# Performance work log

Hardware: AMD Instinct MI355X
Metric: run time of the kernel (lower is better)

Reference implementation:

```python
import jax, jax.numpy as jnp
import numpy as np

L = 8192   # query length
N = 8192   # key/value length
DK = 128   # head dim = dmodel // h = 2048 // 16
PAD = 128  # number of trailing padded key positions


def setup_inputs() -> dict:
    key = jax.random.key(0)
    kq, kk, kv = jax.random.split(key, 3)
    Q = jax.random.normal(kq, (L, DK), dtype=jnp.float32)
    K = jax.random.normal(kk, (N, DK), dtype=jnp.float32)
    V = jax.random.normal(kv, (N, DK), dtype=jnp.float32)
    # True = masked. Causal mask (strict upper triangle) for self-attention.
    mask_self_attention = ~jnp.tril(jnp.ones((L, N), dtype=bool))
    # Padding mask: last PAD key positions are padding.
    mask_padding = jnp.zeros((L, N), dtype=bool).at[:, N - PAD:].set(True)
    return {"Q": Q, "K": K, "V": V,
            "mask_self_attention": mask_self_attention,
            "mask_padding": mask_padding}


def reference(Q, K, V, mask_self_attention, mask_padding):
    # SDPA(Q,K,V) = softmax(QK^T / sqrt(dk)) V ; dropout is identity in eval.
    scale = 1.0 / np.sqrt(DK).astype(np.float32)
    scores = (Q @ K.T) * scale                       # [L, N]
    scores = jnp.where(mask_self_attention, -jnp.inf, scores)
    scores = jnp.where(mask_padding, -jnp.inf, scores)
    attn = jax.nn.softmax(scores, axis=-1)           # [L, N]
    return attn @ V                                   # [L, DK]
```

## Files before the change

kernel.cpp:

```cpp
#include <hip/hip_runtime.h>
#include <stdint.h>

typedef __attribute__((ext_vector_type(8))) short short8;
typedef __attribute__((ext_vector_type(4))) float f32x4;

#define D_K 128
#define N_KV 8192
#define NT 128

__device__ __forceinline__ unsigned short f2bf(float x) {
  unsigned int u = __float_as_uint(x);
  u += 0x7FFFu + ((u >> 16) & 1u);
  return (unsigned short)(u >> 16);
}
__device__ __forceinline__ unsigned int pk2(float lo, float hi) {
  return (unsigned int)f2bf(lo) | ((unsigned int)f2bf(hi) << 16);
}
__device__ __forceinline__ void gload16(const void* g, void* l) {
  __builtin_amdgcn_global_load_lds(
      (const __attribute__((address_space(1))) unsigned int*)g,
      (__attribute__((address_space(3))) unsigned int*)l, 16, 0, 0);
}
__device__ __host__ __forceinline__ int nunits(int t) {
  int n = 2 * t + 2;
  return n > 252 ? 252 : n;
}

__global__ void prep_kernel(const float* __restrict__ Q,
                            const float* __restrict__ K,
                            const float* __restrict__ V,
                            unsigned short* __restrict__ Qb,
                            unsigned short* __restrict__ Kb,
                            unsigned short* __restrict__ Vtb) {
  __shared__ unsigned short tile[64][65];
  const int b = blockIdx.x;
  const int tid = threadIdx.x;
  if (b < 1024) {
    const float scale = (b < 512) ? 0.12751742941349835f : 1.0f;
    const float* src = (b < 512) ? Q : K;
    unsigned short* dst = (b < 512) ? Qb : Kb;
    const int i = (b & 511) * 256 + tid;
    const float4* s = (const float4*)src;
    float4 a = s[2 * i], c4 = s[2 * i + 1];
    uint4 o;
    o.x = pk2(a.x * scale, a.y * scale);
    o.y = pk2(a.z * scale, a.w * scale);
    o.z = pk2(c4.x * scale, c4.y * scale);
    o.w = pk2(c4.z * scale, c4.w * scale);
    *(uint4*)(dst + (size_t)i * 8) = o;
  } else {
    const int bb = b - 1024;
    const int kv0 = (bb >> 1) << 6, dk0 = (bb & 1) << 6;
    const int r = tid >> 2;
    const int c0 = (tid & 3) << 4;
#pragma unroll
    for (int j = 0; j < 4; ++j) {
      float4 v = *(const float4*)(V + (size_t)(kv0 + r) * D_K + dk0 + c0 + 4 * j);
      tile[r][c0 + 4 * j + 0] = f2bf(v.x);
      tile[r][c0 + 4 * j + 1] = f2bf(v.y);
      tile[r][c0 + 4 * j + 2] = f2bf(v.z);
      tile[r][c0 + 4 * j + 3] = f2bf(v.w);
    }
    __syncthreads();
    __align__(16) unsigned short tmp[16];
#pragma unroll
    for (int j = 0; j < 16; ++j) tmp[j] = tile[c0 + j][r];
    unsigned short* o = Vtb + (size_t)(dk0 + r) * N_KV + kv0 + c0;
    *(uint4*)(o) = *(uint4*)(tmp);
    *(uint4*)(o + 8) = *(uint4*)(tmp + 8);
  }
}

__global__ __launch_bounds__(256, 3) void attn_kernel(
    const unsigned short* __restrict__ Qb,
    const unsigned short* __restrict__ Kb,
    const unsigned short* __restrict__ Vtb,
    float* __restrict__ Opart,
    float2* __restrict__ MLpart,
    int U) {
  int rem = blockIdx.x, t = NT - 1;
  for (;; --t) {
    int nb = (nunits(t) + U - 1) / U;
    if (rem < nb) break;
    rem -= nb;
  }
  const int s = rem;
  const int q0 = t << 6;
  const int n = nunits(t);
  const int u0 = s * U;
  const int u1 = min(u0 + U, n);
  const int slot = blockIdx.x;
  const int tid = threadIdx.x;
  const int lane = tid & 63;
  const int w = tid >> 6;
  const int c = lane & 15;
  const int g = lane >> 4;
  const int qw = q0 + (w << 4);

  __shared__ __align__(16) char lds[49152];

  short8 qf[4];
  {
    const char* qrow = (const char*)(Qb + (size_t)(qw + c) * D_K);
#pragma unroll
    for (int kc = 0; kc < 4; ++kc)
      qf[kc] = *(const short8*)(qrow + kc * 64 + g * 16);
  }

  f32x4 acc[8] = {};
  float m2 = -3e38f, lsum = 0.f;
  const int swp = (c & 3) << 4;

  int kcst[2], vcst[2], ldk[2], ldv[2];
#pragma unroll
  for (int ii = 0; ii < 2; ++ii) {
    const int ck = 2 * w + ii;
    const int rowK = (ck << 2) + (lane >> 4);
    kcst[ii] = rowK * 256 + (((lane & 15) << 4) ^ ((rowK & 7) << 4));
    ldk[ii] = ck << 10;
    const int rowV = (ck << 4) + (lane >> 2);
    vcst[ii] = rowV * 16384 + (((lane & 3) << 4) ^ ((rowV & 3) << 4));
    ldv[ii] = 8192 + (ck << 10);
  }
  auto stage = [&](int u, int b) {
    char* base = lds + b * 16384;
    const int koff = (u << 5) * 256;
    const int voff = (u << 5) * 2;
#pragma unroll
    for (int ii = 0; ii < 2; ++ii) {
      gload16((const char*)Kb + koff + kcst[ii], base + ldk[ii]);
      gload16((const char*)Vtb + voff + vcst[ii], base + ldv[ii]);
    }
  };

  stage(u0, 0);
  if (u0 + 1 < u1) stage(u0 + 1, 1);
  int cb = 0;
  for (int u = u0; u < u1; ++u) {
    if (u + 1 < u1) asm volatile("s_waitcnt vmcnt(4)" ::: "memory");
    else            asm volatile("s_waitcnt vmcnt(0)" ::: "memory");
    __builtin_amdgcn_s_barrier();
    asm volatile("" ::: "memory");
    if (u + 2 < u1) {
      int nb2 = cb + 2; if (nb2 >= 3) nb2 -= 3;
      stage(u + 2, nb2);
    }
    const int kv0 = u << 5;
    char* const Kl = lds + cb * 16384;
    char* const Vl = Kl + 8192;

    if (kv0 <= qw + 15) {
      f32x4 st[2] = {};
      __builtin_amdgcn_s_setprio(1);
#pragma unroll
      for (int tt = 0; tt < 2; ++tt) {
        const int krow = (tt << 4) + c;
        const char* kbase = Kl + krow * 256;
        const int swk = (krow & 7) << 4;
#pragma unroll
        for (int kc = 0; kc < 4; ++kc) {
          short8 kf = *(const short8*)(kbase + ((kc * 64 + g * 16) ^ swk));
          st[tt] = __builtin_amdgcn_mfma_f32_16x16x32_bf16(kf, qf[kc], st[tt], 0, 0, 0);
        }
      }
      __builtin_amdgcn_s_setprio(0);
#pragma unroll
      for (int tt = 0; tt < 2; ++tt) {
        if (kv0 + (tt << 4) + 15 > qw) {
          const int kvb = kv0 + (tt << 4) + (g << 2);
#pragma unroll
          for (int r = 0; r < 4; ++r)
            if (kvb + r > qw + c) st[tt][r] = -__builtin_inff();
        }
      }
      float mx = fmaxf(fmaxf(fmaxf(st[0][0], st[0][1]), fmaxf(st[0][2], st[0][3])),
                       fmaxf(fmaxf(st[1][0], st[1][1]), fmaxf(st[1][2], st[1][3])));
      mx = fmaxf(mx, __shfl_xor(mx, 16));
      mx = fmaxf(mx, __shfl_xor(mx, 32));
      if (!__all(mx <= m2 + 8.0f)) {
        const float m2new = fmaxf(m2, mx);
        const float alpha = exp2f(m2 - m2new);
        lsum *= alpha;
#pragma unroll
        for (int r = 0; r < 4; ++r) {
          const float fr = __shfl(alpha, (g << 2) + r);
#pragma unroll
          for (int d = 0; d < 8; ++d) acc[d][r] *= fr;
        }
        m2 = m2new;
      }
      float p[8], psum = 0.f;
#pragma unroll
      for (int tt = 0; tt < 2; ++tt)
#pragma unroll
        for (int r = 0; r < 4; ++r) {
          const float v = exp2f(st[tt][r] - m2);
          p[(tt << 2) + r] = v;
          psum += v;
        }
      psum += __shfl_xor(psum, 16);
      psum += __shfl_xor(psum, 32);
      lsum += psum;
      unsigned int wv0 = pk2(p[0], p[1]), wv1 = pk2(p[2], p[3]);
      unsigned int wv2 = pk2(p[4], p[5]), wv3 = pk2(p[6], p[7]);
      const bool hi = (g >> 1) != 0;
      const int srcb = c + ((g & 1) << 5);
      union { unsigned int u4[4]; short8 s8; } pu;
      {
        const unsigned int a0 = (unsigned int)__shfl((int)wv0, srcb);
        const unsigned int b0 = (unsigned int)__shfl((int)wv2, srcb);
        const unsigned int a1 = (unsigned int)__shfl((int)wv1, srcb);
        const unsigned int b1 = (unsigned int)__shfl((int)wv3, srcb);
        const unsigned int a2 = (unsigned int)__shfl((int)wv0, srcb + 16);
        const unsigned int b2 = (unsigned int)__shfl((int)wv2, srcb + 16);
        const unsigned int a3 = (unsigned int)__shfl((int)wv1, srcb + 16);
        const unsigned int b3 = (unsigned int)__shfl((int)wv3, srcb + 16);
        pu.u4[0] = hi ? b0 : a0;
        pu.u4[1] = hi ? b1 : a1;
        pu.u4[2] = hi ? b2 : a2;
        pu.u4[3] = hi ? b3 : a3;
      }
      const short8 pa = pu.s8;
      __builtin_amdgcn_s_setprio(1);
#pragma unroll
      for (int d = 0; d < 8; ++d) {
        const short8 vb = *(const short8*)(Vl + (d << 10) + c * 64 + ((g << 4) ^ swp));
        acc[d] = __builtin_amdgcn_mfma_f32_16x16x32_bf16(pa, vb, acc[d], 0, 0, 0);
      }
      __builtin_amdgcn_s_setprio(0);
    }
    if (++cb == 3) cb = 0;
  }

  float* op = Opart + (size_t)slot * 8192 + (size_t)(w << 4) * 128;
#pragma unroll
  for (int d = 0; d < 8; ++d)
#pragma unroll
    for (int r = 0; r < 4; ++r)
      op[((g << 2) + r) * 128 + (d << 4) + c] = acc[d][r];
  if (lane < 16)
    MLpart[slot * 64 + (w << 4) + lane] = make_float2(m2, lsum);
}

__global__ void combine_kernel(const float* __restrict__ Opart,
                               const float2* __restrict__ MLpart,
                               float* __restrict__ Out, int U) {
  const int gidx = blockIdx.x * 256 + threadIdx.x;
  const int q = gidx >> 5;
  const int cb = (gidx & 31) << 2;
  const int t = q >> 6, rl = q & 63;
  const int ns = (nunits(t) + U - 1) / U;
  int base = 0;
  for (int tt = NT - 1; tt > t; --tt) base += (nunits(tt) + U - 1) / U;

  float M = -3e38f;
  for (int s2 = 0; s2 < ns; ++s2)
    M = fmaxf(M, MLpart[(base + s2) * 64 + rl].x);
  float nx = 0, ny = 0, nz = 0, nw = 0, den = 0;
  for (int s2 = 0; s2 < ns; ++s2) {
    const float2 ml = MLpart[(base + s2) * 64 + rl];
    if (ml.x > -1e37f) {
      const float wg = exp2f(ml.x - M);
      den += ml.y * wg;
      const float4 o = *(const float4*)(Opart + (size_t)(base + s2) * 8192 + rl * 128 + cb);
      nx += wg * o.x; ny += wg * o.y; nz += wg * o.z; nw += wg * o.w;
    }
  }
  const float inv = 1.f / den;
  float4 r; r.x = nx * inv; r.y = ny * inv; r.z = nz * inv; r.w = nw * inv;
  *(float4*)(Out + (size_t)q * 128 + cb) = r;
}

extern "C" void kernel_launch(void* const* d_in, const int* in_sizes, int n_in,
                              void* d_out, int out_size, void* d_ws, size_t ws_size,
                              hipStream_t stream) {
  (void)in_sizes; (void)n_in; (void)out_size;
  const float* Q = (const float*)d_in[0];
  const float* K = (const float*)d_in[1];
  const float* V = (const float*)d_in[2];
  float* out = (float*)d_out;
  char* ws = (char*)d_ws;

  int U = 2;
  long slots = 0;
  for (;;) {
    slots = 0;
    for (int t = 0; t < NT; ++t) slots += (nunits(t) + U - 1) / U;
    size_t need = (size_t)(8u << 20) + (size_t)slots * 64 * 128 * 4;
    if ((slots <= 768 && need <= ws_size) || U >= 252) break;
    ++U;
  }

  unsigned short* Qb  = (unsigned short*)(ws);
  unsigned short* Kb  = (unsigned short*)(ws + (1u << 21));
  unsigned short* Vtb = (unsigned short*)(ws + (2u << 21));
  float2* MLp = (float2*)(ws + (3u << 21));
  float*  Op  = (float*)(ws + (8u << 20));

  prep_kernel<<<1280, 256, 0, stream>>>(Q, K, V, Qb, Kb, Vtb);
  attn_kernel<<<(int)slots, 256, 0, stream>>>(Qb, Kb, Vtb, Op, MLp, U);
  combine_kernel<<<1024, 256, 0, stream>>>(Op, MLp, out, U);
}
```

Measured before the change: 80.83 us.

## Compute transposed PV product to drop P shuffles, use hardware bf16 pack

```diff
diff --git a/kernel.cpp b/kernel.cpp
--- a/kernel.cpp
+++ b/kernel.cpp
@@ -2,6 +2,7 @@
 #include <stdint.h>
 
 typedef __attribute__((ext_vector_type(8))) short short8;
+typedef __attribute__((ext_vector_type(4))) short s16x4;
 typedef __attribute__((ext_vector_type(4))) float f32x4;
 
 #define D_K 128
@@ -15,6 +16,15 @@
 }
 __device__ __forceinline__ unsigned int pk2(float lo, float hi) {
   return (unsigned int)f2bf(lo) | ((unsigned int)f2bf(hi) << 16);
+}
+__device__ __forceinline__ unsigned int cvtpk(float lo, float hi) {
+  unsigned int r;
+  asm("v_cvt_pk_bf16_f32 %0, %1, %2" : "=v"(r) : "v"(lo), "v"(hi));
+  return r;
+}
+__device__ __forceinline__ f32x4 mfma16(s16x4 a, s16x4 b, f32x4 c) {
+  asm("v_mfma_f32_16x16x16_bf16 %0, %1, %2, %0" : "+v"(c) : "v"(a), "v"(b));
+  return c;
 }
 __device__ __forceinline__ void gload16(const void* g, void* l) {
   __builtin_amdgcn_global_load_lds(
@@ -107,9 +117,11 @@
       qf[kc] = *(const short8*)(qrow + kc * 64 + g * 16);
   }
 
-  f32x4 acc[8] = {};
+  f32x4 accT[8] = {};
   float m2 = -3e38f, lsum = 0.f;
   const int swp = (c & 3) << 4;
+  const int vo0 = (g << 3) ^ swp;
+  const int vo1 = (32 + (g << 3)) ^ swp;
 
   int kcst[2], vcst[2], ldk[2], ldv[2];
 #pragma unroll
@@ -182,11 +194,9 @@
         const float alpha = exp2f(m2 - m2new);
         lsum *= alpha;
 #pragma unroll
-        for (int r = 0; r < 4; ++r) {
-          const float fr = __shfl(alpha, (g << 2) + r);
-#pragma unroll
-          for (int d = 0; d < 8; ++d) acc[d][r] *= fr;
-        }
+        for (int d = 0; d < 8; ++d)
+#pragma unroll
+          for (int r = 0; r < 4; ++r) accT[d][r] *= alpha;
         m2 = m2new;
       }
       float p[8], psum = 0.f;
@@ -201,43 +211,29 @@
       psum += __shfl_xor(psum, 16);
       psum += __shfl_xor(psum, 32);
       lsum += psum;
-      unsigned int wv0 = pk2(p[0], p[1]), wv1 = pk2(p[2], p[3]);
-      unsigned int wv2 = pk2(p[4], p[5]), wv3 = pk2(p[6], p[7]);
-      const bool hi = (g >> 1) != 0;
-      const int srcb = c + ((g & 1) << 5);
-      union { unsigned int u4[4]; short8 s8; } pu;
-      {
-        const unsigned int a0 = (unsigned int)__shfl((int)wv0, srcb);
-        const unsigned int b0 = (unsigned int)__shfl((int)wv2, srcb);
-        const unsigned int a1 = (unsigned int)__shfl((int)wv1, srcb);
-        const unsigned int b1 = (unsigned int)__shfl((int)wv3, srcb);
-        const unsigned int a2 = (unsigned int)__shfl((int)wv0, srcb + 16);
-        const unsigned int b2 = (unsigned int)__shfl((int)wv2, srcb + 16);
-        const unsigned int a3 = (unsigned int)__shfl((int)wv1, srcb + 16);
-        const unsigned int b3 = (unsigned int)__shfl((int)wv3, srcb + 16);
-        pu.u4[0] = hi ? b0 : a0;
-        pu.u4[1] = hi ? b1 : a1;
-        pu.u4[2] = hi ? b2 : a2;
-        pu.u4[3] = hi ? b3 : a3;
-      }
-      const short8 pa = pu.s8;
+      union { unsigned int u2[2]; s16x4 s4; } pb0, pb1;
+      pb0.u2[0] = cvtpk(p[0], p[1]);
+      pb0.u2[1] = cvtpk(p[2], p[3]);
+      pb1.u2[0] = cvtpk(p[4], p[5]);
+      pb1.u2[1] = cvtpk(p[6], p[7]);
       __builtin_amdgcn_s_setprio(1);
 #pragma unroll
       for (int d = 0; d < 8; ++d) {
-        const short8 vb = *(const short8*)(Vl + (d << 10) + c * 64 + ((g << 4) ^ swp));
-        acc[d] = __builtin_amdgcn_mfma_f32_16x16x32_bf16(pa, vb, acc[d], 0, 0, 0);
+        const char* vrow = Vl + (d << 10) + c * 64;
+        const s16x4 va0 = *(const s16x4*)(vrow + vo0);
+        const s16x4 va1 = *(const s16x4*)(vrow + vo1);
+        accT[d] = mfma16(va0, pb0.s4, accT[d]);
+        accT[d] = mfma16(va1, pb1.s4, accT[d]);
       }
       __builtin_amdgcn_s_setprio(0);
     }
     if (++cb == 3) cb = 0;
   }
 
-  float* op = Opart + (size_t)slot * 8192 + (size_t)(w << 4) * 128;
+  float* op = Opart + (size_t)slot * 8192 + (size_t)((w << 4) + c) * 128 + (g << 2);
 #pragma unroll
   for (int d = 0; d < 8; ++d)
-#pragma unroll
-    for (int r = 0; r < 4; ++r)
-      op[((g << 2) + r) * 128 + (d << 4) + c] = acc[d][r];
+    *(f32x4*)(op + (d << 4)) = accT[d];
   if (lane < 16)
     MLpart[slot * 64 + (w << 4) + lane] = make_float2(m2, lsum);
 }
```

Measured after the change: 93.47 us. 1.16x slower.
